# Kernel tuning notes

Measured on AMD Instinct MI355X. Metric: run time of the kernel, lower is better.

Reference implementation:

```python
import jax, jax.numpy as jnp
import numpy as np

HS, FF, NH = 1024, 4096, 16
HD = HS // NH
EPS = 1e-5

def _ln(x, g, b):
    m = jnp.mean(x, axis=-1, keepdims=True)
    v = jnp.mean((x - m) ** 2, axis=-1, keepdims=True)
    return (x - m) * jax.lax.rsqrt(v + EPS) * g + b

def setup_inputs() -> dict:
    key = jax.random.key(0)
    ks = jax.random.split(key, 12)
    s = 1.0 / np.sqrt(HS)
    si = 1.0 / np.sqrt(FF)
    d = {
        "hidden_states": jax.random.normal(ks[0], (2, 2048, HS), dtype=jnp.float32),
        "attention_mask": jnp.zeros((2, 1, 1, 2048), dtype=jnp.float32),
        "Wq": jax.random.uniform(ks[1], (HS, HS), minval=-s, maxval=s),
        "bq": jnp.zeros((HS,), jnp.float32),
        "Wk": jax.random.uniform(ks[2], (HS, HS), minval=-s, maxval=s),
        "bk": jnp.zeros((HS,), jnp.float32),
        "Wv": jax.random.uniform(ks[3], (HS, HS), minval=-s, maxval=s),
        "bv": jnp.zeros((HS,), jnp.float32),
        "Wo": jax.random.uniform(ks[4], (HS, HS), minval=-s, maxval=s),
        "bo": jnp.zeros((HS,), jnp.float32),
        "W1": jax.random.uniform(ks[5], (HS, FF), minval=-s, maxval=s),
        "b1": jnp.zeros((FF,), jnp.float32),
        "W2": jax.random.uniform(ks[6], (FF, HS), minval=-si, maxval=si),
        "b2": jnp.zeros((HS,), jnp.float32),
        "ln1_g": jnp.ones((HS,), jnp.float32),
        "ln1_b": jnp.zeros((HS,), jnp.float32),
        "ln2_g": jnp.ones((HS,), jnp.float32),
        "ln2_b": jnp.zeros((HS,), jnp.float32),
    }
    return d

def reference(hidden_states, attention_mask, Wq, bq, Wk, bk, Wv, bv, Wo, bo,
              W1, b1, W2, b2, ln1_g, ln1_b, ln2_g, ln2_b):
    bs, S, _ = hidden_states.shape
    x = hidden_states
    # self-attention (dropout is identity in eval)
    q = (x @ Wq + bq).reshape(bs, S, NH, HD).transpose(0, 2, 1, 3)
    k = (x @ Wk + bk).reshape(bs, S, NH, HD).transpose(0, 2, 1, 3)
    v = (x @ Wv + bv).reshape(bs, S, NH, HD).transpose(0, 2, 1, 3)
    scores = jnp.einsum("bhqd,bhkd->bhqk", q, k) / np.sqrt(HD) + attention_mask
    probs = jax.nn.softmax(scores, axis=-1)
    attn = jnp.einsum("bhqk,bhkd->bhqd", probs, v)
    attn = attn.transpose(0, 2, 1, 3).reshape(bs, S, HS)
    mha = attn @ Wo + bo
    h = _ln(x + mha, ln1_g, ln1_b)
    # FFN
    ff = jax.nn.relu(h @ W1 + b1) @ W2 + b2
    return _ln(h + ff, ln2_g, ln2_b)
```

## Files before the change

### kernel.cpp

```cpp
#include <hip/hip_runtime.h>
#include <hip/hip_bf16.h>

#define HS   1024
#define FF   4096
#define NH   16
#define HD   64
#define SEQ  2048
#define BSZ  2
#define MROWS (BSZ * SEQ)
#define EPS  1e-5f
#define QKV_STRIDE (3 * HS)

typedef float f32x4  __attribute__((ext_vector_type(4)));
typedef short bf16x8 __attribute__((ext_vector_type(8)));

#if __has_builtin(__builtin_amdgcn_exp2f)
#define EXP2(x) __builtin_amdgcn_exp2f(x)
#else
#define EXP2(x) exp2f(x)
#endif

__device__ __forceinline__ unsigned short f2bf(float x) {
  unsigned int u = __float_as_uint(x);
  u += 0x7fffu + ((u >> 16) & 1u);
  return (unsigned short)(u >> 16);
}

__device__ __forceinline__ float bf2f(unsigned short u) {
  return __uint_as_float((unsigned int)u << 16);
}

__device__ __forceinline__ unsigned int pkbf(float a, float b) {
  union { __hip_bfloat162 h; unsigned int u; } x;
  x.h = __float22bfloat162_rn(float2{a, b});
  return x.u;
}

__device__ __forceinline__ void async16(const ushort* g, ushort* lds) {
  __builtin_amdgcn_global_load_lds(
      (const __attribute__((address_space(1))) unsigned int*)g,
      (__attribute__((address_space(3))) unsigned int*)lds, 16, 0, 0);
}

#define BARSB { __builtin_amdgcn_s_barrier(); __builtin_amdgcn_sched_barrier(0); }

#define QUAD(kt, MH, NH)                                                      \
  {                                                                           \
    const ushort* As_ = &smem[(size_t)((kt) & 1) * 32768];                    \
    const ushort* Bs_ = As_ + 16384;                                          \
    bf16x8 af[4][2], bfr[2][2];                                               \
    _Pragma("unroll")                                                         \
    for (int mt = 0; mt < 4; ++mt)                                            \
      _Pragma("unroll")                                                       \
      for (int s = 0; s < 2; ++s) {                                           \
        const int m = wr * 128 + (MH) * 64 + mt * 16 + lr;                    \
        af[mt][s] = *(const bf16x8*)&As_[(size_t)m * 64 +                     \
                                         (((s * 4 + lg) ^ (m & 7)) * 8)];     \
      }                                                                       \
    _Pragma("unroll")                                                         \
    for (int nj = 0; nj < 2; ++nj)                                            \
      _Pragma("unroll")                                                       \
      for (int s = 0; s < 2; ++s) {                                           \
        const int n = wc * 64 + (NH) * 32 + nj * 16 + lr;                     \
        bfr[nj][s] = *(const bf16x8*)&Bs_[(size_t)n * 64 +                    \
                                          (((s * 4 + lg) ^ (n & 7)) * 8)];    \
      }                                                                       \
    __builtin_amdgcn_s_setprio(1);                                            \
    _Pragma("unroll")                                                         \
    for (int s = 0; s < 2; ++s)                                               \
      _Pragma("unroll")                                                       \
      for (int mt = 0; mt < 4; ++mt)                                          \
        _Pragma("unroll")                                                     \
        for (int nj = 0; nj < 2; ++nj)                                        \
          acc[(MH) * 4 + mt][(NH) * 2 + nj] =                                 \
              __builtin_amdgcn_mfma_f32_16x16x32_bf16(                        \
                  af[mt][s], bfr[nj][s], acc[(MH) * 4 + mt][(NH) * 2 + nj],   \
                  0, 0, 0);                                                   \
    __builtin_amdgcn_s_setprio(0);                                            \
  }

template <bool RELU>
__global__ __launch_bounds__(512, 2) void gemm8_bf16_kernel(
    const ushort* __restrict__ A, const ushort* __restrict__ Bt,
    const float* __restrict__ bias, ushort* __restrict__ C,
    int M, int N, int K)
{
  __shared__ ushort smem[65536];
  const int tid = threadIdx.x;
  const int wv = tid >> 6, ln = tid & 63;
  const int wr = wv >> 2, wc = wv & 3;
  const int lr = ln & 15, lg = ln >> 4;
  const int rr = ln >> 3, cc = ln & 7;

  const unsigned nxy = gridDim.x * gridDim.y;
  unsigned id = blockIdx.y * gridDim.x + blockIdx.x;
  id = (id & 7) * (nxy >> 3) + (id >> 3);
  const int bn = id % gridDim.x, bm = id / gridDim.x;

  f32x4 acc[8][4];
#pragma unroll
  for (int i = 0; i < 8; ++i)
#pragma unroll
    for (int j = 0; j < 4; ++j) acc[i][j] = (f32x4){0.f, 0.f, 0.f, 0.f};

  auto stA = [&](int kt, int h) {
#pragma unroll
    for (int u = 0; u < 2; ++u) {
      const int tt = h + u * 2;
      const int R = tt * 64 + wv * 8 + rr;
      async16(A + (size_t)(bm * 256 + R) * K + kt * 64 + ((cc ^ (R & 7)) * 8),
              &smem[(size_t)(kt & 1) * 32768 + (size_t)(tt * 64 + wv * 8) * 64]);
    }
  };
  auto stB = [&](int kt, int h) {
#pragma unroll
    for (int u = 0; u < 2; ++u) {
      const int tt = h * 2 + u;
      const int R = tt * 64 + wv * 8 + rr;
      async16(Bt + (size_t)(bn * 256 + R) * K + kt * 64 + ((cc ^ (R & 7)) * 8),
              &smem[(size_t)(kt & 1) * 32768 + 16384 + (size_t)(tt * 64 + wv * 8) * 64]);
    }
  };

  stA(0, 0); stA(0, 1); stB(0, 0); stB(0, 1); stA(1, 0);

  const int nIter = K >> 7;
  for (int j = 0; j < nIter; ++j) {
    const int t0 = 2 * j, t1 = t0 + 1;
    const bool nx = (j + 1 < nIter);
    BARSB;
    stA(t1, 1);
    asm volatile("s_waitcnt vmcnt(4)" ::: "memory");
    BARSB;
    QUAD(t0, 0, 0);
    BARSB; stB(t1, 0); QUAD(t0, 0, 1);
    BARSB; if (nx) stA(t0 + 2, 0); QUAD(t0, 1, 0);
    BARSB; stB(t1, 1); QUAD(t0, 1, 1);
    BARSB;
    if (nx) {
      stA(t0 + 2, 1);
      asm volatile("s_waitcnt vmcnt(2)" ::: "memory");
    } else {
      asm volatile("s_waitcnt vmcnt(0)" ::: "memory");
    }
    BARSB;
    QUAD(t1, 0, 0);
    BARSB; if (nx) stB(t0 + 2, 0); QUAD(t1, 0, 1);
    BARSB; if (nx) stB(t0 + 2, 1); QUAD(t1, 1, 0);
    BARSB; if (nx) stA(t0 + 3, 0); QUAD(t1, 1, 1);
  }

  const int gm0 = bm * 256 + wr * 128;
  const int gn0 = bn * 256 + wc * 64;
  float bs4[4];
#pragma unroll
  for (int j = 0; j < 4; ++j) bs4[j] = bias[gn0 + j * 16 + lr];
#pragma unroll
  for (int i = 0; i < 8; ++i) {
#pragma unroll
    for (int r = 0; r < 4; ++r) {
      const size_t row = (size_t)(gm0 + i * 16 + lg * 4 + r);
#pragma unroll
      for (int j = 0; j < 4; ++j) {
        float val = acc[i][j][r] + bs4[j];
        if (RELU) val = fmaxf(val, 0.f);
        C[row * N + gn0 + j * 16 + lr] = f2bf(val);
      }
    }
  }
}

template <int TBM, int TBN, bool RELU, bool OUT_BF16, bool PARTIAL>
__global__ __launch_bounds__(256) void gemm_bf16_kernel(
    const ushort* __restrict__ A, const ushort* __restrict__ Bt,
    const float* __restrict__ bias, void* __restrict__ Cout,
    int M, int N, int K, int kLen, size_t zstride)
{
  constexpr int MI = TBM / 32;
  constexpr int NJ = TBN / 32;
  __shared__ ushort As[TBM * 64];
  __shared__ ushort Bs[TBN * 64];

  const int tid = threadIdx.x;
  const int wv = tid >> 6, ln = tid & 63;

  const unsigned nxy = gridDim.x * gridDim.y;
  unsigned id = blockIdx.y * gridDim.x + blockIdx.x;
  id = (id & 7) * (nxy >> 3) + (id >> 3);
  const int bn = id % gridDim.x, bm = id / gridDim.x;

  const int lr = ln & 15;
  const int lg = ln >> 4;
  const int mrow_base = (wv >> 1) * (TBM / 2);
  const int ncol_base = (wv & 1) * (TBN / 2);

  f32x4 acc[MI][NJ];
#pragma unroll
  for (int i = 0; i < MI; ++i)
#pragma unroll
    for (int j = 0; j < NJ; ++j) acc[i][j] = (f32x4){0.f, 0.f, 0.f, 0.f};

  const int rr = ln >> 3, cc = ln & 7;
  const int kBeg = blockIdx.z * kLen, kEnd = kBeg + kLen;

  for (int k0 = kBeg; k0 < kEnd; k0 += 64) {
    __syncthreads();
#pragma unroll
    for (int t = 0; t < TBM / 32; ++t) {
      const int R = wv * (TBM / 4) + t * 8 + rr;
      const int c = cc ^ (R & 7);
      async16(A + (size_t)(bm * TBM + R) * K + k0 + c * 8,
              &As[(size_t)(wv * (TBM / 4) + t * 8) * 64]);
    }
#pragma unroll
    for (int t = 0; t < TBN / 32; ++t) {
      const int R = wv * (TBN / 4) + t * 8 + rr;
      const int c = cc ^ (R & 7);
      async16(Bt + (size_t)(bn * TBN + R) * K + k0 + c * 8,
              &Bs[(size_t)(wv * (TBN / 4) + t * 8) * 64]);
    }
    __syncthreads();

#pragma unroll
    for (int s = 0; s < 2; ++s) {
      bf16x8 a[MI], b[NJ];
#pragma unroll
      for (int i = 0; i < MI; ++i) {
        const int m = mrow_base + i * 16 + lr;
        a[i] = *(const bf16x8*)&As[(size_t)m * 64 + (((s * 4 + lg) ^ (m & 7)) * 8)];
      }
#pragma unroll
      for (int j = 0; j < NJ; ++j) {
        const int n = ncol_base + j * 16 + lr;
        b[j] = *(const bf16x8*)&Bs[(size_t)n * 64 + (((s * 4 + lg) ^ (n & 7)) * 8)];
      }
#pragma unroll
      for (int i = 0; i < MI; ++i)
#pragma unroll
        for (int j = 0; j < NJ; ++j)
          acc[i][j] = __builtin_amdgcn_mfma_f32_16x16x32_bf16(a[i], b[j], acc[i][j], 0, 0, 0);
    }
  }

  const int gm0 = bm * TBM + mrow_base;
  const int gn0 = bn * TBN + ncol_base;

  if (PARTIAL) {
    float* Cp = (float*)Cout + (size_t)blockIdx.z * zstride;
#pragma unroll
    for (int i = 0; i < MI; ++i)
#pragma unroll
      for (int r = 0; r < 4; ++r) {
        const size_t row = (size_t)(gm0 + i * 16 + lg * 4 + r);
#pragma unroll
        for (int j = 0; j < NJ; ++j)
          Cp[row * N + gn0 + j * 16 + lr] = acc[i][j][r];
      }
  } else {
    float bs4[NJ];
#pragma unroll
    for (int j = 0; j < NJ; ++j) bs4[j] = bias[gn0 + j * 16 + lr];
    float* Cf = (float*)Cout;
    ushort* Cb = (ushort*)Cout;
#pragma unroll
    for (int i = 0; i < MI; ++i) {
#pragma unroll
      for (int r = 0; r < 4; ++r) {
        const size_t row = (size_t)(gm0 + i * 16 + lg * 4 + r);
#pragma unroll
        for (int j = 0; j < NJ; ++j) {
          float val = acc[i][j][r] + bs4[j];
          if (RELU) val = fmaxf(val, 0.f);
          const size_t idx = row * N + gn0 + j * 16 + lr;
          if (OUT_BF16) Cb[idx] = f2bf(val);
          else          Cf[idx] = val;
        }
      }
    }
  }
}

__device__ __forceinline__ void transpose_tile(
    const float* __restrict__ W, ushort* __restrict__ Wt,
    int K, int N, int n0, int k0, int tid, ushort (*T)[72])
{
#pragma unroll
  for (int t = 0; t < 4; ++t) {
    const int r = t * 16 + (tid >> 4);
    const int c = (tid & 15) * 4;
    const float4 w = *(const float4*)&W[(size_t)(k0 + r) * N + n0 + c];
    T[c + 0][r] = f2bf(w.x); T[c + 1][r] = f2bf(w.y);
    T[c + 2][r] = f2bf(w.z); T[c + 3][r] = f2bf(w.w);
  }
  __syncthreads();
#pragma unroll
  for (int t = 0; t < 4; ++t) {
    const int n = t * 16 + (tid >> 4);
    const int kc = (tid & 15) * 4;
    ushort4 o;
    o.x = T[n][kc]; o.y = T[n][kc + 1]; o.z = T[n][kc + 2]; o.w = T[n][kc + 3];
    *(ushort4*)&Wt[(size_t)(n0 + n) * K + k0 + kc] = o;
  }
}

__global__ __launch_bounds__(256) void prep_kernel(
    const float* __restrict__ Wq, const float* __restrict__ Wk,
    const float* __restrict__ Wv, const float* __restrict__ Wo,
    const float* __restrict__ W1, const float* __restrict__ W2,
    const float* __restrict__ bq, const float* __restrict__ bk,
    const float* __restrict__ bv, const float* __restrict__ x,
    const float* __restrict__ mask,
    ushort* __restrict__ Wqkvt, ushort* __restrict__ Wot,
    ushort* __restrict__ W1t, ushort* __restrict__ W2t,
    float* __restrict__ bqkv, ushort* __restrict__ xb,
    float* __restrict__ maskL2)
{
  __shared__ ushort T[64][72];
  const int b = blockIdx.x, tid = threadIdx.x;
  const size_t M1 = 1024 * 1024;
  if (b < 1024) {
    const int w = b >> 8, l = b & 255;
    const int n0 = (l & 15) * 64, k0 = (l >> 4) * 64;
    const float* src = (w == 0) ? Wq : (w == 1) ? Wk : (w == 2) ? Wv : Wo;
    ushort* dst = (w < 3) ? (Wqkvt + (size_t)w * M1) : Wot;
    transpose_tile(src, dst, HS, HS, n0, k0, tid, T);
  } else if (b < 2048) {
    const int l = b - 1024;
    transpose_tile(W1, W1t, HS, FF, (l & 63) * 64, (l >> 6) * 64, tid, T);
  } else if (b < 3072) {
    const int l = b - 2048;
    transpose_tile(W2, W2t, FF, HS, (l & 15) * 64, (l >> 4) * 64, tid, T);
  } else if (b < 5120) {
    const size_t base = (size_t)(b - 3072) * 2048 + tid * 8;
    const float4 v0 = *(const float4*)&x[base];
    const float4 v1 = *(const float4*)&x[base + 4];
    ushort4 o0, o1;
    o0.x = f2bf(v0.x); o0.y = f2bf(v0.y); o0.z = f2bf(v0.z); o0.w = f2bf(v0.w);
    o1.x = f2bf(v1.x); o1.y = f2bf(v1.y); o1.z = f2bf(v1.z); o1.w = f2bf(v1.w);
    *(ushort4*)&xb[base] = o0;
    *(ushort4*)&xb[base + 4] = o1;
  } else {
#pragma unroll
    for (int t = 0; t < 12; ++t) {
      const int i = t * 256 + tid;
      bqkv[i] = (i < HS) ? bq[i] : (i < 2 * HS) ? bk[i - HS] : bv[i - 2 * HS];
    }
#pragma unroll
    for (int t = 0; t < 16; ++t) {
      const int i = t * 256 + tid;
      maskL2[i] = mask[i] * 1.44269504f;
    }
  }
}

__global__ __launch_bounds__(256) void vtrans_kernel(
    const ushort* __restrict__ vb, ushort* __restrict__ VTg, int stride)
{
  __shared__ ushort T[64][68];
  const int tid = threadIdx.x;
  const int s0 = blockIdx.x * 64;
  const int bh = blockIdx.y;
  const int b = bh >> 4, h = bh & 15;
#pragma unroll
  for (int t = 0; t < 4; ++t) {
    const int rr = t * 16 + (tid >> 4);
    const int c4 = (tid & 15) * 4;
    const ushort4 w = *(const ushort4*)&vb[(size_t)(b * SEQ + s0 + rr) * stride + h * 64 + c4];
    T[c4 + 0][rr] = w.x; T[c4 + 1][rr] = w.y;
    T[c4 + 2][rr] = w.z; T[c4 + 3][rr] = w.w;
  }
  __syncthreads();
#pragma unroll
  for (int t = 0; t < 4; ++t) {
    const int d = t * 16 + (tid >> 4);
    const int k4 = (tid & 15) * 4;
    ushort4 o;
    o.x = T[d][k4]; o.y = T[d][k4 + 1]; o.z = T[d][k4 + 2]; o.w = T[d][k4 + 3];
    *(ushort4*)&VTg[((size_t)bh * 64 + d) * SEQ + s0 + k4] = o;
  }
}

__global__ __launch_bounds__(512, 2) void attention_mfma_kernel(
    const ushort* __restrict__ Qb, const ushort* __restrict__ Kb,
    const ushort* __restrict__ VTg, const float* __restrict__ maskL2,
    ushort* __restrict__ O)
{
  __shared__ ushort smem[69632];
  float* mL = (float*)(smem + 65536);

  const int tid = threadIdx.x;
  const int wv = tid >> 6, ln = tid & 63;
  const int c = ln & 15, g = ln >> 4;

  const unsigned d0 = blockIdx.x + 8u * (blockIdx.y + 16u * blockIdx.z);
  const unsigned w0 = (d0 & 7) * 32 + (d0 >> 3);
  const int qt = w0 & 7;
  const int hh = (w0 >> 3) & 15;
  const int b  = w0 >> 7;

  const int bh = b * NH + hh;
  const size_t row0 = (size_t)b * SEQ + (size_t)qt * 256;
  const int ch = hh * HD;
  const int wq0 = wv * 32;

  bf16x8 qf[2][2];
#pragma unroll
  for (int nt = 0; nt < 2; ++nt)
#pragma unroll
    for (int s = 0; s < 2; ++s)
      qf[nt][s] = *(const bf16x8*)&Qb[(row0 + wq0 + nt * 16 + c) * QKV_STRIDE + ch + s * 32 + g * 8];

  const float* mrow = maskL2 + (size_t)b * SEQ;
  async16((const ushort*)(mrow + wv * 256 + ln * 4), (ushort*)(mL + wv * 256));

  const int rr = ln >> 3, cc = ln & 7;
  const int r4 = ln >> 4, sc = ln & 15;

  auto stage = [&](int kb, int bsel) {
    ushort* Ks  = smem + bsel * 16384;
    ushort* VTs = Ks + 8192;
    const size_t krow0 = (size_t)b * SEQ + (size_t)kb * 128;
#pragma unroll
    for (int t = 0; t < 2; ++t) {
      const int r = wv * 16 + t * 8 + rr;
      async16(Kb + (krow0 + r) * QKV_STRIDE + ch + ((cc ^ (r & 7)) * 8),
              &Ks[(size_t)(wv * 16 + t * 8) * 64]);
    }
#pragma unroll
    for (int t = 0; t < 2; ++t) {
      const int d = wv * 8 + t * 4 + r4;
      const int srcc = (sc & 8) | ((sc & 7) ^ (d & 7));
      async16(VTg + ((size_t)bh * 64 + d) * SEQ + kb * 128 + srcc * 8,
              &VTs[(size_t)(wv * 8 + t * 4) * 128]);
    }
  };

  f32x4 ao[4][2];
#pragma unroll
  for (int i = 0; i < 4; ++i) { ao[i][0] = (f32x4){0,0,0,0}; ao[i][1] = (f32x4){0,0,0,0}; }
  float l_r[2] = {0.f, 0.f};

  stage(0, 0);
  stage(1, 1);

  constexpr int NT = SEQ / 128;
  for (int kb = 0; kb < NT; ++kb) {
    const int cur = kb & 3;
    if (kb + 2 < NT) stage(kb + 2, (kb + 2) & 3);
    if (kb + 2 < NT)      asm volatile("s_waitcnt vmcnt(8)" ::: "memory");
    else if (kb + 1 < NT) asm volatile("s_waitcnt vmcnt(4)" ::: "memory");
    else                  asm volatile("s_waitcnt vmcnt(0)" ::: "memory");
    __builtin_amdgcn_s_barrier();
    __builtin_amdgcn_sched_barrier(0);

    ushort* Ks  = smem + cur * 16384;
    ushort* VTs = Ks + 8192;

    f32x4 as_[8][2];
#pragma unroll
    for (int i = 0; i < 8; ++i) { as_[i][0] = (f32x4){0,0,0,0}; as_[i][1] = (f32x4){0,0,0,0}; }
    __builtin_amdgcn_s_setprio(1);
#pragma unroll
    for (int s = 0; s < 2; ++s) {
#pragma unroll
      for (int mt = 0; mt < 8; ++mt) {
        const int key = mt * 16 + c;
        const bf16x8 kf = *(const bf16x8*)&Ks[(size_t)key * 64 + (((s * 4 + g) ^ (key & 7)) * 8)];
#pragma unroll
        for (int nt = 0; nt < 2; ++nt)
          as_[mt][nt] = __builtin_amdgcn_mfma_f32_16x16x32_bf16(kf, qf[nt][s], as_[mt][nt], 0, 0, 0);
      }
    }
    __builtin_amdgcn_s_setprio(0);

#pragma unroll
    for (int mt = 0; mt < 8; ++mt) {
      const float4 mk = *(const float4*)&mL[kb * 128 + mt * 16 + g * 4];
      const float mka[4] = {mk.x, mk.y, mk.z, mk.w};
#pragma unroll
      for (int nt = 0; nt < 2; ++nt) {
#pragma unroll
        for (int r = 0; r < 4; ++r) {
          const float p = EXP2(fmaf(as_[mt][nt][r], 0.18033688f, mka[r]));
          as_[mt][nt][r] = p;
          l_r[nt] += p;
        }
      }
    }

#pragma unroll
    for (int s = 0; s < 4; ++s) {
      bf16x8 pf[2];
#pragma unroll
      for (int nt = 0; nt < 2; ++nt) {
        const unsigned A0 = pkbf(as_[2 * s][nt][0], as_[2 * s][nt][1]);
        const unsigned A1 = pkbf(as_[2 * s][nt][2], as_[2 * s][nt][3]);
        const unsigned B0 = pkbf(as_[2 * s + 1][nt][0], as_[2 * s + 1][nt][1]);
        const unsigned B1 = pkbf(as_[2 * s + 1][nt][2], as_[2 * s + 1][nt][3]);
        auto x0 = __builtin_amdgcn_permlane32_swap(A0, B0, false, false);
        auto x1 = __builtin_amdgcn_permlane32_swap(A1, B1, false, false);
        auto y0 = __builtin_amdgcn_permlane16_swap(x0[0], x0[1], false, false);
        auto y1 = __builtin_amdgcn_permlane16_swap(x1[0], x1[1], false, false);
        union { unsigned w[4]; bf16x8 v; } u;
        u.w[0] = y0[0]; u.w[1] = y1[0]; u.w[2] = y0[1]; u.w[3] = y1[1];
        pf[nt] = u.v;
      }
      __builtin_amdgcn_s_setprio(1);
#pragma unroll
      for (int mt = 0; mt < 4; ++mt) {
        const int d = mt * 16 + c;
        const int k = s * 4 + g;
        const int vslot = (k & 8) | ((k & 7) ^ (d & 7));
        const bf16x8 vf = *(const bf16x8*)&VTs[(size_t)d * 128 + vslot * 8];
#pragma unroll
        for (int nt = 0; nt < 2; ++nt)
          ao[mt][nt] = __builtin_amdgcn_mfma_f32_16x16x32_bf16(vf, pf[nt], ao[mt][nt], 0, 0, 0);
      }
      __builtin_amdgcn_s_setprio(0);
    }
  }

#pragma unroll
  for (int nt = 0; nt < 2; ++nt) {
    l_r[nt] += __shfl_xor(l_r[nt], 16, 64);
    l_r[nt] += __shfl_xor(l_r[nt], 32, 64);
  }

  __syncthreads();
  ushort* OL = smem;
#pragma unroll
  for (int nt = 0; nt < 2; ++nt) {
    const float inv = 1.f / l_r[nt];
    const int q = wq0 + nt * 16 + c;
#pragma unroll
    for (int mt = 0; mt < 4; ++mt) {
      const int d = mt * 16 + g * 4;
      uint2 w;
      w.x = pkbf(ao[mt][nt][0] * inv, ao[mt][nt][1] * inv);
      w.y = pkbf(ao[mt][nt][2] * inv, ao[mt][nt][3] * inv);
      *(uint2*)&OL[q * 72 + d] = w;
    }
  }
  __syncthreads();
#pragma unroll
  for (int it = 0; it < 4; ++it) {
    const int unit = it * 512 + tid;
    const int q = unit >> 3, sg = unit & 7;
    const uint4 w = *(const uint4*)&OL[q * 72 + sg * 8];
    *(uint4*)&O[(row0 + q) * HS + ch + sg * 8] = w;
  }
}

template <bool EMIT16>
__global__ __launch_bounds__(256) void add_ln_red_kernel(
    const float* __restrict__ P0, const float* __restrict__ P1,
    const float* __restrict__ bias, const float* __restrict__ X,
    const float* __restrict__ g, const float* __restrict__ b,
    float* __restrict__ out, ushort* __restrict__ outb)
{
  const int row = blockIdx.x;
  const int tid = threadIdx.x;
  const size_t base = (size_t)row * HS + tid * 4;
  const float4 p0 = *(const float4*)&P0[base];
  const float4 p1 = *(const float4*)&P1[base];
  const float4 bi = *(const float4*)&bias[tid * 4];
  const float4 xv = *(const float4*)&X[base];
  float4 v;
  v.x = xv.x + p0.x + p1.x + bi.x;
  v.y = xv.y + p0.y + p1.y + bi.y;
  v.z = xv.z + p0.z + p1.z + bi.z;
  v.w = xv.w + p0.w + p1.w + bi.w;
  float s1 = v.x + v.y + v.z + v.w;
  float s2 = v.x * v.x + v.y * v.y + v.z * v.z + v.w * v.w;
#pragma unroll
  for (int off = 32; off > 0; off >>= 1) {
    s1 += __shfl_down(s1, off, 64);
    s2 += __shfl_down(s2, off, 64);
  }
  __shared__ float red[8];
  __shared__ float stat[2];
  const int wid = tid >> 6;
  if ((tid & 63) == 0) { red[wid] = s1; red[4 + wid] = s2; }
  __syncthreads();
  if (tid == 0) {
    const float t1 = red[0] + red[1] + red[2] + red[3];
    const float t2 = red[4] + red[5] + red[6] + red[7];
    const float mean = t1 * (1.f / HS);
    const float var = t2 * (1.f / HS) - mean * mean;
    stat[0] = mean;
    stat[1] = rsqrtf(var + EPS);
  }
  __syncthreads();
  const float mean = stat[0], rstd = stat[1];
  const float4 gv = *(const float4*)&g[tid * 4];
  const float4 bv = *(const float4*)&b[tid * 4];
  float4 r;
  r.x = (v.x - mean) * rstd * gv.x + bv.x;
  r.y = (v.y - mean) * rstd * gv.y + bv.y;
  r.z = (v.z - mean) * rstd * gv.z + bv.z;
  r.w = (v.w - mean) * rstd * gv.w + bv.w;
  *(float4*)&out[base] = r;
  if (EMIT16) {
    ushort4 o;
    o.x = f2bf(r.x); o.y = f2bf(r.y); o.z = f2bf(r.z); o.w = f2bf(r.w);
    *(ushort4*)&outb[base] = o;
  }
}

__global__ __launch_bounds__(256) void add_ln_bf16_kernel(
    const ushort* __restrict__ Pb, const float* __restrict__ X,
    const float* __restrict__ g, const float* __restrict__ b,
    float* __restrict__ out, ushort* __restrict__ outb)
{
  const int row = blockIdx.x;
  const int tid = threadIdx.x;
  const size_t base = (size_t)row * HS + tid * 4;
  const ushort4 pb = *(const ushort4*)&Pb[base];
  const float4 xv = *(const float4*)&X[base];
  float4 v;
  v.x = xv.x + bf2f(pb.x);
  v.y = xv.y + bf2f(pb.y);
  v.z = xv.z + bf2f(pb.z);
  v.w = xv.w + bf2f(pb.w);
  float s1 = v.x + v.y + v.z + v.w;
  float s2 = v.x * v.x + v.y * v.y + v.z * v.z + v.w * v.w;
#pragma unroll
  for (int off = 32; off > 0; off >>= 1) {
    s1 += __shfl_down(s1, off, 64);
    s2 += __shfl_down(s2, off, 64);
  }
  __shared__ float red[8];
  __shared__ float stat[2];
  const int wid = tid >> 6;
  if ((tid & 63) == 0) { red[wid] = s1; red[4 + wid] = s2; }
  __syncthreads();
  if (tid == 0) {
    const float t1 = red[0] + red[1] + red[2] + red[3];
    const float t2 = red[4] + red[5] + red[6] + red[7];
    const float mean = t1 * (1.f / HS);
    const float var = t2 * (1.f / HS) - mean * mean;
    stat[0] = mean;
    stat[1] = rsqrtf(var + EPS);
  }
  __syncthreads();
  const float mean = stat[0], rstd = stat[1];
  const float4 gv = *(const float4*)&g[tid * 4];
  const float4 bv = *(const float4*)&b[tid * 4];
  float4 r;
  r.x = (v.x - mean) * rstd * gv.x + bv.x;
  r.y = (v.y - mean) * rstd * gv.y + bv.y;
  r.z = (v.z - mean) * rstd * gv.z + bv.z;
  r.w = (v.w - mean) * rstd * gv.w + bv.w;
  *(float4*)&out[base] = r;
  ushort4 o;
  o.x = f2bf(r.x); o.y = f2bf(r.y); o.z = f2bf(r.z); o.w = f2bf(r.w);
  *(ushort4*)&outb[base] = o;
}

extern "C" void kernel_launch(void* const* d_in, const int* in_sizes, int n_in,
                              void* d_out, int out_size, void* d_ws, size_t ws_size,
                              hipStream_t stream)
{
  const float* x    = (const float*)d_in[0];
  const float* mask = (const float*)d_in[1];
  const float* Wq   = (const float*)d_in[2];  const float* bq  = (const float*)d_in[3];
  const float* Wk   = (const float*)d_in[4];  const float* bk  = (const float*)d_in[5];
  const float* Wv   = (const float*)d_in[6];  const float* bv  = (const float*)d_in[7];
  const float* Wo   = (const float*)d_in[8];  const float* bo  = (const float*)d_in[9];
  const float* W1   = (const float*)d_in[10]; const float* b1  = (const float*)d_in[11];
  const float* W2   = (const float*)d_in[12]; const float* b2  = (const float*)d_in[13];
  const float* g1   = (const float*)d_in[14]; const float* be1 = (const float*)d_in[15];
  const float* g2   = (const float*)d_in[16]; const float* be2 = (const float*)d_in[17];
  float* out = (float*)d_out;

  ushort* wsu = (ushort*)d_ws;
  const size_t M1 = 1024 * 1024;

  ushort* Wqkvt = wsu;
  ushort* Wot   = wsu + 3 * M1;
  ushort* W1t   = wsu + 4 * M1;
  ushort* W2t   = wsu + 8 * M1;
  float*  bqkv  = (float*)(wsu + 12 * M1);
  float*  maskL2= (float*)(wsu + 12 * M1 + 8192);
  ushort* xb    = wsu + 13 * M1;
  ushort* qkvb  = wsu + 17 * M1;
  ushort* VTg   = wsu + 29 * M1;
  ushort* attnb = wsu + 33 * M1;
  ushort* mhab  = wsu + 13 * M1;
  float*  h     = (float*)(wsu + 29 * M1);
  ushort* hb    = wsu + 37 * M1;
  ushort* ff1o  = wsu + 13 * M1;
  float*  ff2P0 = (float*)wsu;
  float*  ff2P1 = (float*)(wsu + 39 * M1);

  const dim3 blk(256);

  prep_kernel<<<dim3(5121), blk, 0, stream>>>(
      Wq, Wk, Wv, Wo, W1, W2, bq, bk, bv, x, mask,
      Wqkvt, Wot, W1t, W2t, bqkv, xb, maskL2);

  gemm8_bf16_kernel<false><<<dim3(12, 16), dim3(512), 0, stream>>>(
      xb, Wqkvt, bqkv, qkvb, MROWS, 3 * HS, HS);

  vtrans_kernel<<<dim3(SEQ / 64, BSZ * NH), blk, 0, stream>>>(qkvb + 2 * HS, VTg, QKV_STRIDE);

  attention_mfma_kernel<<<dim3(SEQ / 256, NH, BSZ), dim3(512), 0, stream>>>(
      qkvb, qkvb + HS, VTg, maskL2, attnb);

  gemm_bf16_kernel<64, 128, false, true, false><<<dim3(8, 64), blk, 0, stream>>>(
      attnb, Wot, bo, mhab, MROWS, HS, HS, HS, 0);
  add_ln_bf16_kernel<<<dim3(MROWS), blk, 0, stream>>>(
      mhab, x, g1, be1, h, hb);

  gemm8_bf16_kernel<true><<<dim3(16, 16), dim3(512), 0, stream>>>(
      hb, W1t, b1, ff1o, MROWS, FF, HS);

  gemm_bf16_kernel<128, 128, false, false, true><<<dim3(8, 32, 2), blk, 0, stream>>>(
      ff1o, W2t, nullptr, ff2P0, MROWS, HS, FF, FF / 2, (size_t)(ff2P1 - ff2P0));
  add_ln_red_kernel<false><<<dim3(MROWS), blk, 0, stream>>>(
      ff2P0, ff2P1, b2, h, g2, be2, out, nullptr);
}
```

Measured before the change: 341.3 us.

## Fuse V transpose into QKV GEMM, compute softmax sums via MFMA, retile Wo GEMM

The QKV GEMM epilogue now writes the V columns straight into the transposed per-head VTg layout, so the separate vtrans kernel launch and its extra global round trip go away. In attention, the softmax row sums are no longer accumulated with scalar adds plus cross-lane shuffles. They come from an extra MFMA of a ones vector against the bf16 probabilities, which moves the work to the matrix unit but sums bf16-rounded values. The output-projection GEMM switches from 64x128 to 128x128 tiles, giving fewer, larger blocks.

```diff
diff --git a/kernel.cpp b/kernel.cpp
--- a/kernel.cpp
+++ b/kernel.cpp
@@ -79,11 +79,11 @@
     __builtin_amdgcn_s_setprio(0);                                            \
   }
 
-template <bool RELU>
+template <bool RELU, bool VTRANS>
 __global__ __launch_bounds__(512, 2) void gemm8_bf16_kernel(
     const ushort* __restrict__ A, const ushort* __restrict__ Bt,
     const float* __restrict__ bias, ushort* __restrict__ C,
-    int M, int N, int K)
+    ushort* __restrict__ VTg, int M, int N, int K)
 {
   __shared__ ushort smem[65536];
   const int tid = threadIdx.x;
@@ -155,16 +155,36 @@
   float bs4[4];
 #pragma unroll
   for (int j = 0; j < 4; ++j) bs4[j] = bias[gn0 + j * 16 + lr];
-#pragma unroll
-  for (int i = 0; i < 8; ++i) {
-#pragma unroll
-    for (int r = 0; r < 4; ++r) {
-      const size_t row = (size_t)(gm0 + i * 16 + lg * 4 + r);
+
+  if (VTRANS && gn0 >= 2 * HS) {
+#pragma unroll
+    for (int i = 0; i < 8; ++i) {
 #pragma unroll
       for (int j = 0; j < 4; ++j) {
-        float val = acc[i][j][r] + bs4[j];
-        if (RELU) val = fmaxf(val, 0.f);
-        C[row * N + gn0 + j * 16 + lr] = f2bf(val);
+        const int col = gn0 - 2 * HS + j * 16 + lr;
+        const int rowb = gm0 + i * 16 + lg * 4;
+        const int bb = rowb >> 11;
+        const int seq = rowb & (SEQ - 1);
+        ushort4 o;
+        o.x = f2bf(acc[i][j][0] + bs4[j]);
+        o.y = f2bf(acc[i][j][1] + bs4[j]);
+        o.z = f2bf(acc[i][j][2] + bs4[j]);
+        o.w = f2bf(acc[i][j][3] + bs4[j]);
+        *(ushort4*)&VTg[((size_t)(bb * NH + (col >> 6)) * 64 + (col & 63)) * SEQ + seq] = o;
+      }
+    }
+  } else {
+#pragma unroll
+    for (int i = 0; i < 8; ++i) {
+#pragma unroll
+      for (int r = 0; r < 4; ++r) {
+        const size_t row = (size_t)(gm0 + i * 16 + lg * 4 + r);
+#pragma unroll
+        for (int j = 0; j < 4; ++j) {
+          float val = acc[i][j][r] + bs4[j];
+          if (RELU) val = fmaxf(val, 0.f);
+          C[row * N + gn0 + j * 16 + lr] = f2bf(val);
+        }
       }
     }
   }
@@ -353,33 +373,6 @@
   }
 }
 
-__global__ __launch_bounds__(256) void vtrans_kernel(
-    const ushort* __restrict__ vb, ushort* __restrict__ VTg, int stride)
-{
-  __shared__ ushort T[64][68];
-  const int tid = threadIdx.x;
-  const int s0 = blockIdx.x * 64;
-  const int bh = blockIdx.y;
-  const int b = bh >> 4, h = bh & 15;
-#pragma unroll
-  for (int t = 0; t < 4; ++t) {
-    const int rr = t * 16 + (tid >> 4);
-    const int c4 = (tid & 15) * 4;
-    const ushort4 w = *(const ushort4*)&vb[(size_t)(b * SEQ + s0 + rr) * stride + h * 64 + c4];
-    T[c4 + 0][rr] = w.x; T[c4 + 1][rr] = w.y;
-    T[c4 + 2][rr] = w.z; T[c4 + 3][rr] = w.w;
-  }
-  __syncthreads();
-#pragma unroll
-  for (int t = 0; t < 4; ++t) {
-    const int d = t * 16 + (tid >> 4);
-    const int k4 = (tid & 15) * 4;
-    ushort4 o;
-    o.x = T[d][k4]; o.y = T[d][k4 + 1]; o.z = T[d][k4 + 2]; o.w = T[d][k4 + 3];
-    *(ushort4*)&VTg[((size_t)bh * 64 + d) * SEQ + s0 + k4] = o;
-  }
-}
-
 __global__ __launch_bounds__(512, 2) void attention_mfma_kernel(
     const ushort* __restrict__ Qb, const ushort* __restrict__ Kb,
     const ushort* __restrict__ VTg, const float* __restrict__ maskL2,
@@ -438,7 +431,10 @@
   f32x4 ao[4][2];
 #pragma unroll
   for (int i = 0; i < 4; ++i) { ao[i][0] = (f32x4){0,0,0,0}; ao[i][1] = (f32x4){0,0,0,0}; }
-  float l_r[2] = {0.f, 0.f};
+  f32x4 aol[2];
+  aol[0] = (f32x4){0,0,0,0}; aol[1] = (f32x4){0,0,0,0};
+  const short oneb = (short)0x3F80;
+  const bf16x8 ones = (bf16x8){oneb, oneb, oneb, oneb, oneb, oneb, oneb, oneb};
 
   stage(0, 0);
   stage(1, 1);
@@ -480,11 +476,8 @@
 #pragma unroll
       for (int nt = 0; nt < 2; ++nt) {
 #pragma unroll
-        for (int r = 0; r < 4; ++r) {
-          const float p = EXP2(fmaf(as_[mt][nt][r], 0.18033688f, mka[r]));
-          as_[mt][nt][r] = p;
-          l_r[nt] += p;
-        }
+        for (int r = 0; r < 4; ++r)
+          as_[mt][nt][r] = EXP2(fmaf(as_[mt][nt][r], 0.18033688f, mka[r]));
       }
     }
 
@@ -516,21 +509,18 @@
         for (int nt = 0; nt < 2; ++nt)
           ao[mt][nt] = __builtin_amdgcn_mfma_f32_16x16x32_bf16(vf, pf[nt], ao[mt][nt], 0, 0, 0);
       }
+#pragma unroll
+      for (int nt = 0; nt < 2; ++nt)
+        aol[nt] = __builtin_amdgcn_mfma_f32_16x16x32_bf16(ones, pf[nt], aol[nt], 0, 0, 0);
       __builtin_amdgcn_s_setprio(0);
     }
-  }
-
-#pragma unroll
-  for (int nt = 0; nt < 2; ++nt) {
-    l_r[nt] += __shfl_xor(l_r[nt], 16, 64);
-    l_r[nt] += __shfl_xor(l_r[nt], 32, 64);
   }
 
   __syncthreads();
   ushort* OL = smem;
 #pragma unroll
   for (int nt = 0; nt < 2; ++nt) {
-    const float inv = 1.f / l_r[nt];
+    const float inv = 1.f / aol[nt][0];
     const int q = wq0 + nt * 16 + c;
 #pragma unroll
     for (int mt = 0; mt < 4; ++mt) {
@@ -699,21 +689,19 @@
       Wq, Wk, Wv, Wo, W1, W2, bq, bk, bv, x, mask,
       Wqkvt, Wot, W1t, W2t, bqkv, xb, maskL2);
 
-  gemm8_bf16_kernel<false><<<dim3(12, 16), dim3(512), 0, stream>>>(
-      xb, Wqkvt, bqkv, qkvb, MROWS, 3 * HS, HS);
-
-  vtrans_kernel<<<dim3(SEQ / 64, BSZ * NH), blk, 0, stream>>>(qkvb + 2 * HS, VTg, QKV_STRIDE);
+  gemm8_bf16_kernel<false, true><<<dim3(12, 16), dim3(512), 0, stream>>>(
+      xb, Wqkvt, bqkv, qkvb, VTg, MROWS, 3 * HS, HS);
 
   attention_mfma_kernel<<<dim3(SEQ / 256, NH, BSZ), dim3(512), 0, stream>>>(
       qkvb, qkvb + HS, VTg, maskL2, attnb);
 
-  gemm_bf16_kernel<64, 128, false, true, false><<<dim3(8, 64), blk, 0, stream>>>(
+  gemm_bf16_kernel<128, 128, false, true, false><<<dim3(8, 32), blk, 0, stream>>>(
       attnb, Wot, bo, mhab, MROWS, HS, HS, HS, 0);
   add_ln_bf16_kernel<<<dim3(MROWS), blk, 0, stream>>>(
       mhab, x, g1, be1, h, hb);
 
-  gemm8_bf16_kernel<true><<<dim3(16, 16), dim3(512), 0, stream>>>(
-      hb, W1t, b1, ff1o, MROWS, FF, HS);
+  gemm8_bf16_kernel<true, false><<<dim3(16, 16), dim3(512), 0, stream>>>(
+      hb, W1t, b1, ff1o, nullptr, MROWS, FF, HS);
 
   gemm_bf16_kernel<128, 128, false, false, true><<<dim3(8, 32, 2), blk, 0, stream>>>(
       ff1o, W2t, nullptr, ff2P0, MROWS, HS, FF, FF / 2, (size_t)(ff2P1 - ff2P0));
```

Measured after the change: 335.2 us. No clear change (-1.8%).
